# Optimization experiments

Measured on AMD Instinct MI355X. Metric: run time of the kernel, lower is better.

Reference implementation:

```python
import jax, jax.numpy as jnp
import numpy as np
import math

N = 3072      # number of graph nodes
D = 256       # in_dim == out_dim
H = 8         # heads
EPS = 1e-5    # LayerNorm eps (torch default)


def _glorot(key, shape):
    fan = shape[-2] + shape[-1]
    std = math.sqrt(6.0 / fan)
    return jax.random.uniform(key, shape, jnp.float32, -std, std)


def layer_norm(x, g, b):
    mu = jnp.mean(x, axis=-1, keepdims=True)
    var = jnp.mean(jnp.square(x - mu), axis=-1, keepdims=True)
    return (x - mu) * jax.lax.rsqrt(var + EPS) * g + b


def setup_inputs() -> dict:
    key = jax.random.key(0)
    ks = jax.random.split(key, 12)
    input_x = jax.random.normal(ks[0], (N, D), jnp.float32)
    # degrees: positive floats in [1, 50)
    deg = 1.0 + 49.0 * jax.random.uniform(ks[1], (N,), jnp.float32)
    WQ = _glorot(ks[2], (H, D, D))
    WK = _glorot(ks[3], (H, D, D))
    WV = _glorot(ks[4], (H, D, D))
    # linears stored as [in, out] (math-equivalent to torch's [out,in] transposed)
    lin_attn_w = _glorot(ks[5], (H * D, D)); lin_attn_b = jnp.zeros((D,), jnp.float32)
    lin_w = _glorot(ks[6], (2 * D, D));       lin_b = jnp.zeros((D,), jnp.float32)
    fnn1_w = _glorot(ks[7], (D, D));          fnn1_b = jnp.zeros((D,), jnp.float32)
    fnn2_w = _glorot(ks[8], (D, D));          fnn2_b = jnp.zeros((D,), jnp.float32)
    ln1_g = jnp.ones((D,), jnp.float32); ln1_b = jnp.zeros((D,), jnp.float32)
    ln2_g = jnp.ones((D,), jnp.float32); ln2_b = jnp.zeros((D,), jnp.float32)
    return dict(input_x=input_x, deg=deg, WQ=WQ, WK=WK, WV=WV,
                lin_attn_w=lin_attn_w, lin_attn_b=lin_attn_b,
                lin_w=lin_w, lin_b=lin_b,
                ln1_g=ln1_g, ln1_b=ln1_b,
                fnn1_w=fnn1_w, fnn1_b=fnn1_b,
                fnn2_w=fnn2_w, fnn2_b=fnn2_b,
                ln2_g=ln2_g, ln2_b=ln2_b)


def reference(input_x, deg, WQ, WK, WV, lin_attn_w, lin_attn_b,
              lin_w, lin_b, ln1_g, ln1_b, fnn1_w, fnn1_b,
              fnn2_w, fnn2_b, ln2_g, ln2_b):
    n = input_x.shape[0]
    # --- multi-head attention over all nodes ---
    Q = jnp.einsum('nd,hde->hne', input_x, WQ)   # [H,N,D]
    K = jnp.einsum('nd,hde->hne', input_x, WK)
    V = jnp.einsum('nd,hde->hne', input_x, WV)
    scores = jnp.einsum('hne,hme->hnm', Q, K)    # [H,N,N]
    # diagonal self-mask: QKT[i] += diag_embed(diag(QKT[i]) - 1e20)
    idx = jnp.arange(n)
    diag_vals = scores[:, idx, idx]
    scores = scores.at[:, idx, idx].add(diag_vals - 1e20)
    attn = jax.nn.softmax(scores / math.sqrt(D), axis=-1)
    attn_x = jnp.einsum('hnm,hme->hne', attn, V)           # [H,N,D]
    attn_cat = jnp.transpose(attn_x, (1, 0, 2)).reshape(n, H * D)
    attn_out = attn_cat @ lin_attn_w + lin_attn_b          # [N,D]
    # --- degree-norm concat + residual + LN ---
    x1 = jnp.concatenate([input_x, attn_out / jnp.sqrt(deg)[:, None]], axis=-1)
    x1 = x1 @ lin_w + lin_b
    x1 = layer_norm(input_x + x1, ln1_g, ln1_b)
    # --- FFN block (dropout inactive at eval) ---
    x2 = jax.nn.relu(x1 @ fnn1_w + fnn1_b)
    x2 = x2 @ fnn2_w + fnn2_b
    return layer_norm(x1 + x2, ln2_g, ln2_b)
```

## Files before the change

kernel.cpp:

```cpp
#include <hip/hip_runtime.h>
#include <hip/hip_bf16.h>
#include <stdint.h>

typedef __bf16 bf16x8_t __attribute__((ext_vector_type(8)));
typedef short  s16x8_t  __attribute__((ext_vector_type(8)));
typedef unsigned short u16x4_t __attribute__((ext_vector_type(4)));
typedef float  f32x4_t __attribute__((ext_vector_type(4)));

#define NTOK 3072
#define NHEAD 8
#define NSPLIT 4

__device__ __forceinline__ unsigned short f2bf(float f) {
  union { float f; uint32_t u; } v; v.f = f;
  uint32_t r = v.u + 0x7fffu + ((v.u >> 16) & 1u);
  return (unsigned short)(r >> 16);
}
__device__ __forceinline__ float bf2f(unsigned short s) {
  union { uint32_t u; float f; } v; v.u = ((uint32_t)s) << 16;
  return v.f;
}

__device__ __forceinline__ void gload_lds16(const void* g, void* lds) {
  __builtin_amdgcn_global_load_lds(
      (const __attribute__((address_space(1))) uint32_t*)g,
      (__attribute__((address_space(3))) uint32_t*)lds, 16, 0, 0);
}

__global__ void prep_all(const float* __restrict__ WQ, const float* __restrict__ WK,
                         const float* __restrict__ WV, const float* __restrict__ law,
                         const float* __restrict__ lw, const float* __restrict__ f1w,
                         const float* __restrict__ f2w, const float* __restrict__ x,
                         unsigned short* __restrict__ qkvwT, unsigned short* __restrict__ lawT,
                         unsigned short* __restrict__ lwT, unsigned short* __restrict__ f1T,
                         unsigned short* __restrict__ f2T, unsigned short* __restrict__ xa) {
  __shared__ float tile[64][65];
  const int id = blockIdx.x;
  const int t = threadIdx.x;
  if (id >= 576) {
    int n0 = (id - 576) * 64;
    int col = (t & 63) * 4;
#pragma unroll
    for (int i = 0; i < 16; ++i) {
      int n = n0 + i * 4 + (t >> 6);
      f32x4_t v = *(const f32x4_t*)(x + (size_t)n * 256 + col);
      u16x4_t o;
#pragma unroll
      for (int j = 0; j < 4; ++j) o[j] = f2bf(v[j]);
      *(u16x4_t*)(xa + (size_t)n * 512 + col) = o;
    }
    return;
  }
  const float* src; unsigned short* dst; int sld, dld, d0, e0;
  if (id < 384) {
    int z = id >> 4, tl = id & 15;
    int op = z >> 3, hh = z & 7;
    src = ((op == 0) ? WQ : (op == 1) ? WK : WV) + (size_t)hh * 65536;
    dst = qkvwT + (size_t)z * 65536;
    sld = 256; dld = 256; d0 = (tl >> 2) * 64; e0 = (tl & 3) * 64;
  } else if (id < 512) {
    int tl = id - 384;
    src = law; dst = lawT; sld = 256; dld = 2048;
    d0 = (tl >> 2) * 64; e0 = (tl & 3) * 64;
  } else if (id < 544) {
    int tl = id - 512;
    src = lw; dst = lwT; sld = 256; dld = 512;
    d0 = (tl >> 2) * 64; e0 = (tl & 3) * 64;
  } else if (id < 560) {
    int tl = id - 544;
    src = f1w; dst = f1T; sld = 256; dld = 256;
    d0 = (tl >> 2) * 64; e0 = (tl & 3) * 64;
  } else {
    int tl = id - 560;
    src = f2w; dst = f2T; sld = 256; dld = 256;
    d0 = (tl >> 2) * 64; e0 = (tl & 3) * 64;
  }
  int tr = t >> 4, tc4 = (t & 15) * 4;
#pragma unroll
  for (int i = 0; i < 4; ++i) {
    int d = i * 16 + tr;
    f32x4_t v = *(const f32x4_t*)(src + (size_t)(d0 + d) * sld + e0 + tc4);
    tile[d][tc4] = v[0]; tile[d][tc4 + 1] = v[1]; tile[d][tc4 + 2] = v[2]; tile[d][tc4 + 3] = v[3];
  }
  __syncthreads();
#pragma unroll
  for (int i = 0; i < 4; ++i) {
    int e = i * 16 + tr;
    u16x4_t o;
#pragma unroll
    for (int j = 0; j < 4; ++j) o[j] = f2bf(tile[tc4 + j][e]);
    *(u16x4_t*)(dst + (size_t)(e0 + e) * dld + d0 + tc4) = o;
  }
}

template <int BM, int BN>
__global__ __launch_bounds__(256, 2) void gemm_kernel(
    const unsigned short* __restrict__ A, int lda,
    const unsigned short* __restrict__ B, int ldb,
    void* __restrict__ Cout, int ldc, int Klen,
    const float* __restrict__ bias,
    const float* __restrict__ resid, int ldr,
    const float* __restrict__ deg, int flags,
    float* __restrict__ part, long pstride) {
  constexpr int WM = BM / 2, WN = BN / 2, FM = WM / 16, FN = WN / 16;
  __shared__ unsigned short As[BM * 32];
  __shared__ unsigned short Bs[BN * 32];
  const int t = threadIdx.x;
  const int w = t >> 6, l = t & 63;
  const int l15 = l & 15, lhi = l >> 4;
  const int row0 = blockIdx.y * BM, col0 = blockIdx.x * BN;
  const int wr = (w >> 1) * WM, wc = (w & 1) * WN;

  f32x4_t acc[FM][FN];
#pragma unroll
  for (int m = 0; m < FM; ++m)
#pragma unroll
    for (int n = 0; n < FN; ++n) acc[m][n] = (f32x4_t){0.f, 0.f, 0.f, 0.f};

  const int srow = l >> 2;
  const int spc  = (l & 3) * 16;
  const int kofs0 = blockIdx.z * Klen;
  const int nkt = Klen >> 5;
  for (int kt = 0; kt < nkt; ++kt) {
    const int koff = kofs0 + kt * 32;
    __syncthreads();
#pragma unroll
    for (int c = w; c < BM / 16; c += 4) {
      int ar = c * 16 + srow;
      int lcb = spc ^ (((ar >> 1) & 3) << 4);
      gload_lds16(A + (size_t)(row0 + ar) * lda + koff + (lcb >> 1), &As[c * 512]);
    }
#pragma unroll
    for (int c = w; c < BN / 16; c += 4) {
      int br = c * 16 + srow;
      int lcb = spc ^ (((br >> 1) & 3) << 4);
      gload_lds16(B + (size_t)(col0 + br) * ldb + koff + (lcb >> 1), &Bs[c * 512]);
    }
    __syncthreads();
    bf16x8_t af[FM], bfr[FN];
#pragma unroll
    for (int m = 0; m < FM; ++m) {
      int ar = wr + m * 16 + l15;
      af[m] = *(const bf16x8_t*)(&As[(ar * 64 + ((lhi * 16) ^ (((ar >> 1) & 3) << 4))) >> 1]);
    }
#pragma unroll
    for (int n = 0; n < FN; ++n) {
      int br = wc + n * 16 + l15;
      bfr[n] = *(const bf16x8_t*)(&Bs[(br * 64 + ((lhi * 16) ^ (((br >> 1) & 3) << 4))) >> 1]);
    }
#pragma unroll
    for (int m = 0; m < FM; ++m)
#pragma unroll
      for (int n = 0; n < FN; ++n)
        acc[m][n] = __builtin_amdgcn_mfma_f32_16x16x32_bf16(af[m], bfr[n], acc[m][n], 0, 0, 0);
  }

  const bool relu = flags & 1, obf = flags & 2, dsc = flags & 4, ppart = flags & 8;
#pragma unroll
  for (int m = 0; m < FM; ++m) {
#pragma unroll
    for (int r = 0; r < 4; ++r) {
      int grow = row0 + wr + m * 16 + lhi * 4 + r;
      float sc = dsc ? rsqrtf(deg[grow]) : 1.0f;
#pragma unroll
      for (int n = 0; n < FN; ++n) {
        int gcol = col0 + wc + n * 16 + l15;
        float v = acc[m][n][r];
        if (ppart) {
          part[(size_t)blockIdx.z * pstride + (size_t)grow * ldc + gcol] = v;
          continue;
        }
        if (bias) v += bias[gcol];
        v *= sc;
        if (resid) v += resid[(size_t)grow * ldr + gcol];
        if (relu) v = fmaxf(v, 0.f);
        if (obf)
          ((unsigned short*)Cout)[(size_t)grow * ldc + gcol] = f2bf(v);
        else
          ((float*)Cout)[(size_t)grow * ldc + gcol] = v;
      }
    }
  }
}

__global__ void attn_reduce(const float* __restrict__ part, const float* __restrict__ lab,
                            const float* __restrict__ deg, unsigned short* __restrict__ xa) {
  int n = blockIdx.x, d = threadIdx.x;
  float s = 0.f;
#pragma unroll
  for (int z = 0; z < 4; ++z) s += part[((size_t)z * NTOK + n) * 256 + d];
  xa[(size_t)n * 512 + 256 + d] = f2bf((s + lab[d]) * rsqrtf(deg[n]));
}

#define VSW(e) ((((((e) >> 1) & 3) ^ (((e) >> 3) & 3))) << 4)
__global__ __launch_bounds__(256, 2) void flash_kernel(
    const unsigned short* __restrict__ qkv, unsigned short* __restrict__ pO,
    float* __restrict__ ml) {
  __shared__ unsigned short Ks[2][32 * 256];
  __shared__ unsigned short Vt[2][256 * 32];
  __shared__ unsigned short Ps[4][16 * 32];
  const int bid = blockIdx.x;
  const int hs = bid % (NHEAD * NSPLIT);
  const int qb = bid / (NHEAD * NSPLIT);
  const int h = hs / NSPLIT;
  const int split = hs % NSPLIT;
  const int q0 = qb * 64;
  const int t = threadIdx.x, w = t >> 6, l = t & 63;
  const int l15 = l & 15, lhi = l >> 4;

  const int vn0 = (t & 7) * 4;
  const int ve0 = (t >> 3) * 8;

  auto issueV = [&](int kv0, s16x8_t rv[4]) {
    const unsigned short* Vg = qkv + (size_t)(kv0 + vn0) * 6144 + 4096 + h * 256 + ve0;
#pragma unroll
    for (int rr = 0; rr < 4; ++rr) rv[rr] = *(const s16x8_t*)(Vg + rr * 6144);
  };
  auto issueK = [&](int kv0, int buf) {
    int rh = l >> 5;
    int pc = (l & 31) * 16;
#pragma unroll
    for (int i = 0; i < 4; ++i) {
      int c = w * 4 + i;
      int kr = c * 2 + rh;
      int lcb = pc ^ ((kr & 7) << 4);
      gload_lds16(qkv + (size_t)(kv0 + kr) * 6144 + 2048 + h * 256 + (lcb >> 1),
                  &Ks[buf][c * 512]);
    }
  };
  auto packV = [&](s16x8_t rv[4], int buf) {
#pragma unroll
    for (int j = 0; j < 8; ++j) {
      int e = ve0 + j;
      uint64_t pk = (uint64_t)(unsigned short)rv[0][j] |
                    ((uint64_t)(unsigned short)rv[1][j] << 16) |
                    ((uint64_t)(unsigned short)rv[2][j] << 32) |
                    ((uint64_t)(unsigned short)rv[3][j] << 48);
      int pb = e * 64 + ((vn0 * 2) ^ VSW(e));
      *(uint64_t*)(&Vt[buf][pb >> 1]) = pk;
    }
  };

  bf16x8_t qf[8];
  {
    const unsigned short* Qb = qkv + (size_t)(q0 + w * 16 + l15) * 6144 + h * 256 + lhi * 8;
#pragma unroll
    for (int kk = 0; kk < 8; ++kk) qf[kk] = *(const bf16x8_t*)(Qb + kk * 32);
  }
  f32x4_t o[16];
#pragma unroll
  for (int et = 0; et < 16; ++et) o[et] = (f32x4_t){0.f, 0.f, 0.f, 0.f};
  float m_run[4] = {-1e30f, -1e30f, -1e30f, -1e30f};
  float l_run[4] = {0.f, 0.f, 0.f, 0.f};

  const int nt0 = split * (96 / NSPLIT), nt1 = nt0 + 96 / NSPLIT;

  {
    s16x8_t rva[4];
    issueV(nt0 * 32, rva);
    issueK(nt0 * 32, 0);
    packV(rva, 0);
  }
  __syncthreads();

  for (int nt = nt0; nt < nt1; ++nt) {
    const int c = (nt - nt0) & 1;
    const int kv0 = nt * 32;
    const bool have_nxt = (nt + 1 < nt1);
    s16x8_t rvb[4];
    if (have_nxt) {
      issueV(kv0 + 32, rvb);
      issueK(kv0 + 32, c ^ 1);
    }

    f32x4_t s[2];
#pragma unroll
    for (int ni = 0; ni < 2; ++ni) s[ni] = (f32x4_t){0.f, 0.f, 0.f, 0.f};
    __builtin_amdgcn_s_setprio(1);
#pragma unroll
    for (int kk = 0; kk < 8; ++kk) {
#pragma unroll
      for (int ni = 0; ni < 2; ++ni) {
        int br = ni * 16 + l15;
        bf16x8_t kb = *(const bf16x8_t*)(&Ks[c][(br * 512 + ((kk * 64 + lhi * 16) ^ ((br & 7) << 4))) >> 1]);
        s[ni] = __builtin_amdgcn_mfma_f32_16x16x32_bf16(qf[kk], kb, s[ni], 0, 0, 0);
      }
    }
    __builtin_amdgcn_s_setprio(0);

    float p[2][4];
    float alpha[4];
#pragma unroll
    for (int r = 0; r < 4; ++r) {
      int grow = q0 + w * 16 + lhi * 4 + r;
      float sv[2];
      float mx = -1e30f;
#pragma unroll
      for (int ni = 0; ni < 2; ++ni) {
        float x = s[ni][r] * 0.0625f;
        if (kv0 + ni * 16 + l15 == grow) x = -1e30f;
        sv[ni] = x;
        mx = fmaxf(mx, x);
      }
#pragma unroll
      for (int msk = 1; msk < 16; msk <<= 1) mx = fmaxf(mx, __shfl_xor(mx, msk));
      float mn = fmaxf(m_run[r], mx);
      alpha[r] = __expf(m_run[r] - mn);
      m_run[r] = mn;
      float ls = 0.f;
#pragma unroll
      for (int ni = 0; ni < 2; ++ni) {
        float pv = __expf(sv[ni] - mn);
        p[ni][r] = pv;
        ls += pv;
      }
#pragma unroll
      for (int msk = 1; msk < 16; msk <<= 1) ls += __shfl_xor(ls, msk);
      l_run[r] = l_run[r] * alpha[r] + ls;
    }
#pragma unroll
    for (int et = 0; et < 16; ++et)
#pragma unroll
      for (int r = 0; r < 4; ++r) o[et][r] *= alpha[r];

    unsigned short* Pw = &Ps[w][0];
#pragma unroll
    for (int ni = 0; ni < 2; ++ni)
#pragma unroll
      for (int r = 0; r < 4; ++r) {
        int prow = lhi * 4 + r;
        int pb = prow * 64 + ((((ni * 16 + l15) * 2)) ^ (((prow >> 1) & 3) << 4));
        Pw[pb >> 1] = f2bf(p[ni][r]);
      }
    bf16x8_t pa = *(const bf16x8_t*)(&Pw[(l15 * 64 + ((lhi * 16) ^ (((l15 >> 1) & 3) << 4))) >> 1]);
    __builtin_amdgcn_s_setprio(1);
#pragma unroll
    for (int et = 0; et < 16; ++et) {
      int er = et * 16 + l15;
      bf16x8_t vb = *(const bf16x8_t*)(&Vt[c][(er * 64 + ((lhi * 16) ^ VSW(er))) >> 1]);
      o[et] = __builtin_amdgcn_mfma_f32_16x16x32_bf16(pa, vb, o[et], 0, 0, 0);
    }
    __builtin_amdgcn_s_setprio(0);

    if (have_nxt) packV(rvb, c ^ 1);
    __syncthreads();
  }

  const size_t sh = (size_t)(split * NHEAD + h);
#pragma unroll
  for (int et = 0; et < 16; ++et)
#pragma unroll
    for (int r = 0; r < 4; ++r) {
      int grow = q0 + w * 16 + lhi * 4 + r;
      pO[(sh * NTOK + grow) * 256 + et * 16 + l15] = f2bf(o[et][r]);
    }
  if (l15 == 0) {
#pragma unroll
    for (int r = 0; r < 4; ++r) {
      int grow = q0 + w * 16 + lhi * 4 + r;
      ml[(sh * NTOK + grow) * 2] = m_run[r];
      ml[(sh * NTOK + grow) * 2 + 1] = l_run[r];
    }
  }
}

__global__ void flash_combine(const unsigned short* __restrict__ pO,
                              const float* __restrict__ ml,
                              unsigned short* __restrict__ acat) {
  int n = blockIdx.x, t = threadIdx.x;
  int h = t >> 5, e0 = (t & 31) * 8;
  float ms[NSPLIT], ls[NSPLIT];
  float M = -1e30f;
#pragma unroll
  for (int s = 0; s < NSPLIT; ++s) {
    size_t b = ((size_t)(s * NHEAD + h) * NTOK + n) * 2;
    ms[s] = ml[b]; ls[s] = ml[b + 1];
    M = fmaxf(M, ms[s]);
  }
  float den = 0.f;
  float num[8];
#pragma unroll
  for (int j = 0; j < 8; ++j) num[j] = 0.f;
#pragma unroll
  for (int s = 0; s < NSPLIT; ++s) {
    float ws = __expf(ms[s] - M);
    den += ws * ls[s];
    s16x8_t ov = *(const s16x8_t*)(pO + ((size_t)(s * NHEAD + h) * NTOK + n) * 256 + e0);
#pragma unroll
    for (int j = 0; j < 8; ++j) num[j] += ws * bf2f((unsigned short)ov[j]);
  }
  float rden = 1.0f / den;
  s16x8_t out;
#pragma unroll
  for (int j = 0; j < 8; ++j) out[j] = (short)f2bf(num[j] * rden);
  *(s16x8_t*)(acat + (size_t)n * 2048 + h * 256 + e0) = out;
}

__global__ void ln_kernel(const float* __restrict__ u, const float* __restrict__ g,
                          const float* __restrict__ b, float* __restrict__ outf,
                          unsigned short* __restrict__ outb) {
  int row = blockIdx.x * 4 + (threadIdx.x >> 6);
  int l = threadIdx.x & 63;
  const float* ur = u + (size_t)row * 256;
  f32x4_t v = *(const f32x4_t*)(ur + l * 4);
  float s = v[0] + v[1] + v[2] + v[3];
#pragma unroll
  for (int m = 1; m < 64; m <<= 1) s += __shfl_xor(s, m);
  float mu = s * (1.0f / 256.0f);
  f32x4_t d;
  float vs = 0.f;
#pragma unroll
  for (int i = 0; i < 4; ++i) { d[i] = v[i] - mu; vs += d[i] * d[i]; }
#pragma unroll
  for (int m = 1; m < 64; m <<= 1) vs += __shfl_xor(vs, m);
  float rstd = rsqrtf(vs * (1.0f / 256.0f) + 1e-5f);
  f32x4_t gg = *(const f32x4_t*)(g + l * 4);
  f32x4_t bb = *(const f32x4_t*)(b + l * 4);
#pragma unroll
  for (int i = 0; i < 4; ++i) {
    float o = d[i] * rstd * gg[i] + bb[i];
    if (outf) outf[(size_t)row * 256 + l * 4 + i] = o;
    if (outb) outb[(size_t)row * 256 + l * 4 + i] = f2bf(o);
  }
}

extern "C" void kernel_launch(void* const* d_in, const int* in_sizes, int n_in,
                              void* d_out, int out_size, void* d_ws, size_t ws_size,
                              hipStream_t stream) {
  const float* x    = (const float*)d_in[0];
  const float* deg  = (const float*)d_in[1];
  const float* WQ   = (const float*)d_in[2];
  const float* WK   = (const float*)d_in[3];
  const float* WV   = (const float*)d_in[4];
  const float* law  = (const float*)d_in[5];
  const float* lab  = (const float*)d_in[6];
  const float* lw   = (const float*)d_in[7];
  const float* lb   = (const float*)d_in[8];
  const float* ln1g = (const float*)d_in[9];
  const float* ln1b = (const float*)d_in[10];
  const float* f1w  = (const float*)d_in[11];
  const float* f1b  = (const float*)d_in[12];
  const float* f2w  = (const float*)d_in[13];
  const float* f2b  = (const float*)d_in[14];
  const float* ln2g = (const float*)d_in[15];
  const float* ln2b = (const float*)d_in[16];

  char* ws = (char*)d_ws;
  size_t off = 0;
  auto alloc = [&](size_t bytes) {
    void* p = ws + off;
    off += (bytes + 255) & ~(size_t)255;
    return p;
  };
  unsigned short* qkvwT = (unsigned short*)alloc((size_t)6144 * 256 * 2);
  unsigned short* lawT  = (unsigned short*)alloc((size_t)256 * 2048 * 2);
  unsigned short* lwT   = (unsigned short*)alloc((size_t)256 * 512 * 2);
  unsigned short* f1T   = (unsigned short*)alloc((size_t)256 * 256 * 2);
  unsigned short* f2T   = (unsigned short*)alloc((size_t)256 * 256 * 2);
  unsigned short* xa    = (unsigned short*)alloc((size_t)NTOK * 512 * 2);
  unsigned short* qkv   = (unsigned short*)alloc((size_t)NTOK * 6144 * 2);
  unsigned short* acat  = (unsigned short*)alloc((size_t)NTOK * 2048 * 2);
  unsigned short* pO    = (unsigned short*)alloc((size_t)NSPLIT * NHEAD * NTOK * 256 * 2);
  float*          mlp   = (float*)alloc((size_t)NSPLIT * NHEAD * NTOK * 2 * 4);
  float*          apart = (float*)alloc((size_t)4 * NTOK * 256 * 4);
  float*          u1    = (float*)alloc((size_t)NTOK * 256 * 4);
  float*          x1f   = (float*)alloc((size_t)NTOK * 256 * 4);
  unsigned short* x1b   = (unsigned short*)alloc((size_t)NTOK * 256 * 2);
  unsigned short* tb    = (unsigned short*)alloc((size_t)NTOK * 256 * 2);
  float*          u2    = (float*)alloc((size_t)NTOK * 256 * 4);

  prep_all<<<624, 256, 0, stream>>>(WQ, WK, WV, law, lw, f1w, f2w, x,
                                    qkvwT, lawT, lwT, f1T, f2T, xa);

  gemm_kernel<128, 128><<<dim3(48, 24), 256, 0, stream>>>(
      xa, 512, qkvwT, 256, qkv, 6144, 256, nullptr, nullptr, 0, nullptr, 2, nullptr, 0);

  flash_kernel<<<NTOK / 64 * NHEAD * NSPLIT, 256, 0, stream>>>(qkv, pO, mlp);
  flash_combine<<<NTOK, 256, 0, stream>>>(pO, mlp, acat);

  gemm_kernel<64, 64><<<dim3(4, 48, 4), 256, 0, stream>>>(
      acat, 2048, lawT, 2048, nullptr, 256, 512, nullptr, nullptr, 0, nullptr, 8,
      apart, (long)NTOK * 256);
  attn_reduce<<<NTOK, 256, 0, stream>>>(apart, lab, deg, xa);

  gemm_kernel<64, 64><<<dim3(4, 48), 256, 0, stream>>>(
      xa, 512, lwT, 512, u1, 256, 512, lb, x, 256, nullptr, 0, nullptr, 0);
  ln_kernel<<<NTOK / 4, 256, 0, stream>>>(u1, ln1g, ln1b, x1f, x1b);

  gemm_kernel<64, 64><<<dim3(4, 48), 256, 0, stream>>>(
      x1b, 256, f1T, 256, tb, 256, 256, f1b, nullptr, 0, nullptr, 1 | 2, nullptr, 0);
  gemm_kernel<64, 64><<<dim3(4, 48), 256, 0, stream>>>(
      tb, 256, f2T, 256, u2, 256, 256, f2b, x1f, 256, nullptr, 0, nullptr, 0);
  ln_kernel<<<NTOK / 4, 256, 0, stream>>>(u2, ln2g, ln2b, (float*)d_out, nullptr);
}
```

Measured before the change: 393.2 us.

## Single-buffer K/V LDS in flash kernel for higher occupancy; DPP row reductions

Drops the double-buffered K and V LDS tiles to single buffers. This roughly halves the block's LDS footprint so launch bounds can rise from 2 to 3 blocks per CU. The next tile's loads now start only after the QK MFMAs and a barrier, and the V pack waits behind a second barrier. That gives up in-block prefetch overlap in exchange for more resident waves. Separately, the 16-lane max and sum reductions switch from shfl_xor to DPP quad_perm and mirror moves, which should cut LDS-crossbar shuffle cost in the softmax.

```diff
diff --git a/kernel.cpp b/kernel.cpp
--- a/kernel.cpp
+++ b/kernel.cpp
@@ -25,6 +25,27 @@
   __builtin_amdgcn_global_load_lds(
       (const __attribute__((address_space(1))) uint32_t*)g,
       (__attribute__((address_space(3))) uint32_t*)lds, 16, 0, 0);
+}
+
+template <int CTRL>
+__device__ __forceinline__ float dpp_mv(float x) {
+  union { float f; int i; } u; u.f = x;
+  u.i = __builtin_amdgcn_update_dpp(0, u.i, CTRL, 0xf, 0xf, true);
+  return u.f;
+}
+__device__ __forceinline__ float red_max16(float x) {
+  x = fmaxf(x, dpp_mv<0xB1>(x));
+  x = fmaxf(x, dpp_mv<0x4E>(x));
+  x = fmaxf(x, dpp_mv<0x141>(x));
+  x = fmaxf(x, dpp_mv<0x140>(x));
+  return x;
+}
+__device__ __forceinline__ float red_sum16(float x) {
+  x += dpp_mv<0xB1>(x);
+  x += dpp_mv<0x4E>(x);
+  x += dpp_mv<0x141>(x);
+  x += dpp_mv<0x140>(x);
+  return x;
 }
 
 __global__ void prep_all(const float* __restrict__ WQ, const float* __restrict__ WK,
@@ -193,11 +214,11 @@
 }
 
 #define VSW(e) ((((((e) >> 1) & 3) ^ (((e) >> 3) & 3))) << 4)
-__global__ __launch_bounds__(256, 2) void flash_kernel(
+__global__ __launch_bounds__(256, 3) void flash_kernel(
     const unsigned short* __restrict__ qkv, unsigned short* __restrict__ pO,
     float* __restrict__ ml) {
-  __shared__ unsigned short Ks[2][32 * 256];
-  __shared__ unsigned short Vt[2][256 * 32];
+  __shared__ unsigned short Ks[32 * 256];
+  __shared__ unsigned short Vt[256 * 32];
   __shared__ unsigned short Ps[4][16 * 32];
   const int bid = blockIdx.x;
   const int hs = bid % (NHEAD * NSPLIT);
@@ -216,7 +237,7 @@
 #pragma unroll
     for (int rr = 0; rr < 4; ++rr) rv[rr] = *(const s16x8_t*)(Vg + rr * 6144);
   };
-  auto issueK = [&](int kv0, int buf) {
+  auto issueK = [&](int kv0) {
     int rh = l >> 5;
     int pc = (l & 31) * 16;
 #pragma unroll
@@ -225,10 +246,10 @@
       int kr = c * 2 + rh;
       int lcb = pc ^ ((kr & 7) << 4);
       gload_lds16(qkv + (size_t)(kv0 + kr) * 6144 + 2048 + h * 256 + (lcb >> 1),
-                  &Ks[buf][c * 512]);
+                  &Ks[c * 512]);
     }
   };
-  auto packV = [&](s16x8_t rv[4], int buf) {
+  auto packV = [&](s16x8_t rv[4]) {
 #pragma unroll
     for (int j = 0; j < 8; ++j) {
       int e = ve0 + j;
@@ -237,7 +258,7 @@
                     ((uint64_t)(unsigned short)rv[2][j] << 32) |
                     ((uint64_t)(unsigned short)rv[3][j] << 48);
       int pb = e * 64 + ((vn0 * 2) ^ VSW(e));
-      *(uint64_t*)(&Vt[buf][pb >> 1]) = pk;
+      *(uint64_t*)(&Vt[pb >> 1]) = pk;
     }
   };
 
@@ -258,64 +279,54 @@
   {
     s16x8_t rva[4];
     issueV(nt0 * 32, rva);
-    issueK(nt0 * 32, 0);
-    packV(rva, 0);
+    issueK(nt0 * 32);
+    packV(rva);
   }
   __syncthreads();
 
   for (int nt = nt0; nt < nt1; ++nt) {
-    const int c = (nt - nt0) & 1;
     const int kv0 = nt * 32;
     const bool have_nxt = (nt + 1 < nt1);
+
+    f32x4_t s[2];
+#pragma unroll
+    for (int ni = 0; ni < 2; ++ni) s[ni] = (f32x4_t){0.f, 0.f, 0.f, 0.f};
+    __builtin_amdgcn_s_setprio(1);
+#pragma unroll
+    for (int kk = 0; kk < 8; ++kk) {
+#pragma unroll
+      for (int ni = 0; ni < 2; ++ni) {
+        int br = ni * 16 + l15;
+        bf16x8_t kb = *(const bf16x8_t*)(&Ks[(br * 512 + ((kk * 64 + lhi * 16) ^ ((br & 7) << 4))) >> 1]);
+        s[ni] = __builtin_amdgcn_mfma_f32_16x16x32_bf16(qf[kk], kb, s[ni], 0, 0, 0);
+      }
+    }
+    __builtin_amdgcn_s_setprio(0);
+    __syncthreads();
+
     s16x8_t rvb[4];
     if (have_nxt) {
       issueV(kv0 + 32, rvb);
-      issueK(kv0 + 32, c ^ 1);
-    }
-
-    f32x4_t s[2];
-#pragma unroll
-    for (int ni = 0; ni < 2; ++ni) s[ni] = (f32x4_t){0.f, 0.f, 0.f, 0.f};
-    __builtin_amdgcn_s_setprio(1);
-#pragma unroll
-    for (int kk = 0; kk < 8; ++kk) {
-#pragma unroll
-      for (int ni = 0; ni < 2; ++ni) {
-        int br = ni * 16 + l15;
-        bf16x8_t kb = *(const bf16x8_t*)(&Ks[c][(br * 512 + ((kk * 64 + lhi * 16) ^ ((br & 7) << 4))) >> 1]);
-        s[ni] = __builtin_amdgcn_mfma_f32_16x16x32_bf16(qf[kk], kb, s[ni], 0, 0, 0);
-      }
-    }
-    __builtin_amdgcn_s_setprio(0);
+      issueK(kv0 + 32);
+    }
 
     float p[2][4];
     float alpha[4];
 #pragma unroll
     for (int r = 0; r < 4; ++r) {
       int grow = q0 + w * 16 + lhi * 4 + r;
-      float sv[2];
-      float mx = -1e30f;
-#pragma unroll
-      for (int ni = 0; ni < 2; ++ni) {
-        float x = s[ni][r] * 0.0625f;
-        if (kv0 + ni * 16 + l15 == grow) x = -1e30f;
-        sv[ni] = x;
-        mx = fmaxf(mx, x);
-      }
-#pragma unroll
-      for (int msk = 1; msk < 16; msk <<= 1) mx = fmaxf(mx, __shfl_xor(mx, msk));
+      float sv0 = s[0][r] * 0.0625f;
+      float sv1 = s[1][r] * 0.0625f;
+      if (kv0 + l15 == grow) sv0 = -1e30f;
+      if (kv0 + 16 + l15 == grow) sv1 = -1e30f;
+      float mx = red_max16(fmaxf(sv0, sv1));
       float mn = fmaxf(m_run[r], mx);
       alpha[r] = __expf(m_run[r] - mn);
       m_run[r] = mn;
-      float ls = 0.f;
-#pragma unroll
-      for (int ni = 0; ni < 2; ++ni) {
-        float pv = __expf(sv[ni] - mn);
-        p[ni][r] = pv;
-        ls += pv;
-      }
-#pragma unroll
-      for (int msk = 1; msk < 16; msk <<= 1) ls += __shfl_xor(ls, msk);
+      float pv0 = __expf(sv0 - mn);
+      float pv1 = __expf(sv1 - mn);
+      p[0][r] = pv0; p[1][r] = pv1;
+      float ls = red_sum16(pv0 + pv1);
       l_run[r] = l_run[r] * alpha[r] + ls;
     }
 #pragma unroll
@@ -337,13 +348,15 @@
 #pragma unroll
     for (int et = 0; et < 16; ++et) {
       int er = et * 16 + l15;
-      bf16x8_t vb = *(const bf16x8_t*)(&Vt[c][(er * 64 + ((lhi * 16) ^ VSW(er))) >> 1]);
+      bf16x8_t vb = *(const bf16x8_t*)(&Vt[(er * 64 + ((lhi * 16) ^ VSW(er))) >> 1]);
       o[et] = __builtin_amdgcn_mfma_f32_16x16x32_bf16(pa, vb, o[et], 0, 0, 0);
     }
     __builtin_amdgcn_s_setprio(0);
 
-    if (have_nxt) packV(rvb, c ^ 1);
-    __syncthreads();
+    if (have_nxt) {
+      __syncthreads();
+      packV(rvb);
+    }
   }
 
   const size_t sh = (size_t)(split * NHEAD + h);
```

New measurement: 432.2 us. 9.9% more time.
